# Performance work log

Hardware: AMD Instinct MI355X
Metric: run time of the kernel (lower is better)

The kernel has to match this reference:

```python
import jax, jax.numpy as jnp
import numpy as np
jax.config.update("jax_enable_x64", True)

N_ITER = 5
B, N = 64, 128

_C1 = jnp.uint64(0x9E3779B97F4A7C15)
_C2 = jnp.uint64(0xBF58476D1CE4E5B9)
_C3 = jnp.uint64(0x94D049BB133111EB)
_SALT = jnp.uint64(0xD1B54A32D192ED03)


def _mix(x):
    # splitmix64 finalizer: a bijection on uint64 -> preserves label equality classes
    z = x + _C1
    z = (z ^ (z >> jnp.uint64(30))) * _C2
    z = (z ^ (z >> jnp.uint64(27))) * _C3
    return z ^ (z >> jnp.uint64(31))


def setup_inputs() -> dict:
    key = jax.random.key(0)
    k1, k2 = jax.random.split(key)
    u = jax.random.uniform(k1, (B, N, N))
    adj = jnp.where(u < 0.06, 1.0, 0.0).astype(jnp.float32)
    adj = jnp.maximum(adj, jnp.transpose(adj, (0, 2, 1)))  # symmetric
    eye = jnp.eye(N, dtype=jnp.float32)
    adj = adj * (1.0 - eye)  # no self loops
    labels = jax.random.randint(k2, (B, N), 0, 10, dtype=jnp.int32)
    return {"adj": adj, "labels": labels}


def _kernel_contrib(h):
    # h: [B, N] uint64 labels. K[i,j] = #{(u,v): label_u == label_v}
    L = h.reshape(-1)                                   # [T]
    eq = (L[:, None] == L[None, :]).astype(jnp.float32)  # [T, T]
    return eq.reshape(B, N, B, N).sum(axis=(1, 3))       # [B, B]


def reference(adj, labels):
    adj_u = (adj > 0.5).astype(jnp.uint64)        # [B, N, N]
    h = _mix(labels.astype(jnp.uint64))           # initial labels (bijective relabel)
    K = _kernel_contrib(h)
    for _ in range(N_ITER):
        # commutative multiset hash of neighbor labels
        nsum = jnp.einsum('bij,bj->bi', adj_u, _mix(h ^ _SALT))
        # combine own label with neighbor multiset -> WL relabel
        h = _mix(_mix(h) + nsum)
        K = K + _kernel_contrib(h)
    d = jnp.sqrt(jnp.diag(K))
    return K / (d[:, None] * d[None, :])
```

## Files before the change

### kernel.cpp

```cpp
#include <hip/hip_runtime.h>

typedef unsigned long long u64;
typedef unsigned int u32;

#define NB 64
#define NN 128
#define NITER 5
#define NGEN 6
#define SALT 0xD1B54A32D192ED03ULL
#define NPAIR_OFF (NB*(NB-1)/2)
#define TSLOTS 256

__device__ __forceinline__ u64 mix64(u64 x) {
    u64 z = x + 0x9E3779B97F4A7C15ULL;
    z = (z ^ (z >> 30)) * 0xBF58476D1CE4E5B9ULL;
    z = (z ^ (z >> 27)) * 0x94D049BB133111EBULL;
    return z ^ (z >> 31);
}

__global__ __launch_bounds__(512) void wl_stage1(const float* __restrict__ adj,
                                                 const int* __restrict__ labels,
                                                 u64* __restrict__ hgen,
                                                 u64* __restrict__ keysg,
                                                 u32* __restrict__ cntsg,
                                                 float* __restrict__ Kpart,
                                                 float* __restrict__ out) {
    const int blk = blockIdx.x;
    const int t = threadIdx.x;
    const int u = t & 127;
    const int q = t >> 7;
    const bool writer = blk < NB;
    const int b    = writer ? blk   : (blk - NB) / NGEN;
    const int gent = writer ? NITER : (blk - NB) % NGEN;

    __shared__ u64 gsh[NN];
    __shared__ u64 psum[3][NN];
    __shared__ u64 keys[TSLOTS];
    __shared__ u32 cnts[TSLOTS];
    __shared__ u32 part[4];

    u32 m = 0;
    if (gent > 0) {
        const float* rowp = adj + ((size_t)b * NN + u) * NN + q * 32;
        #pragma unroll
        for (int k = 0; k < 8; ++k) {
            const float4 v = *(const float4*)(rowp + 4 * k);
            m |= (v.x > 0.5f ? 1u : 0u) << (4 * k);
            m |= (v.y > 0.5f ? 1u : 0u) << (4 * k + 1);
            m |= (v.z > 0.5f ? 1u : 0u) << (4 * k + 2);
            m |= (v.w > 0.5f ? 1u : 0u) << (4 * k + 3);
        }
    }

    u64 h = 0;
    if (q == 0) {
        h = mix64((u64)(u32)labels[b * NN + u]);
        if (writer) hgen[(size_t)b * (NGEN * NN) + u] = h;
    }

    for (int it = 0; it < gent; ++it) {
        if (q == 0) gsh[u] = mix64(h ^ SALT);
        __syncthreads();
        u64 s = 0;
        {
            u32 mm = m;
            const u64* gp = gsh + q * 32;
            while (mm) { int j = __builtin_ctz(mm); mm &= mm - 1; s += gp[j]; }
        }
        if (q) psum[q - 1][u] = s;
        __syncthreads();
        if (q == 0) {
            h = mix64(mix64(h) + s + psum[0][u] + psum[1][u] + psum[2][u]);
            if (writer) hgen[(size_t)b * (NGEN * NN) + (it + 1) * NN + u] = h;
        }
    }
    if (writer) return;

    if (t < TSLOTS) { keys[t] = 0ULL; cnts[t] = 0u; }
    __syncthreads();
    if (q == 0) {
        u32 s = (u32)h & (TSLOTS - 1);
        for (;;) {
            u64 old = atomicCAS((unsigned long long*)&keys[s], 0ULL, h);
            if (old == 0ULL || old == h) { atomicAdd(&cnts[s], 1u); break; }
            s = (s + 1) & (TSLOTS - 1);
        }
    }
    __syncthreads();

    const int bg = b * NGEN + gent;
    if (t < TSLOTS) {
        const u64 kk = keys[t];
        const u32 cc = cnts[t];
        keysg[(size_t)bg * TSLOTS + t] = kk;
        cntsg[(size_t)bg * TSLOTS + t] = cc;
        u32 acc = cc * cc;
        #pragma unroll
        for (int off = 32; off > 0; off >>= 1) acc += __shfl_down(acc, off);
        if ((t & 63) == 0) part[t >> 6] = acc;
    }
    __syncthreads();
    if (t == 0) {
        Kpart[bg] = (float)(part[0] + part[1] + part[2] + part[3]);
        if (gent == 0) out[b * NB + b] = 1.0f;
    }
}

__global__ __launch_bounds__(256) void wl_pairs(const u64* __restrict__ hgen,
                                                const u64* __restrict__ keysg,
                                                const u32* __restrict__ cntsg,
                                                const float* __restrict__ Kpart,
                                                float* __restrict__ out) {
    const int p = blockIdx.x;
    int b1 = (int)((1.0f + sqrtf(1.0f + 8.0f * (float)p)) * 0.5f);
    while (b1 * (b1 - 1) / 2 > p) --b1;
    while ((b1 + 1) * b1 / 2 <= p) ++b1;
    const int b2 = p - b1 * (b1 - 1) / 2;

    const int t = threadIdx.x;
    __shared__ u64 keys[NGEN * TSLOTS];
    __shared__ u32 cnts[NGEN * TSLOTS];
    __shared__ u32 part[4];
    __shared__ float dred[2 * NGEN];

    if (t < 2 * NGEN)
        dred[t] = Kpart[(t < NGEN ? b1 : b2) * NGEN + (t % NGEN)];

    {
        const ulonglong2* src = (const ulonglong2*)(keysg + (size_t)b2 * NGEN * TSLOTS);
        ulonglong2* dst = (ulonglong2*)keys;
        #pragma unroll
        for (int k = 0; k < 3; ++k) dst[t + 256 * k] = src[t + 256 * k];
    }
    {
        const uint4* src = (const uint4*)(cntsg + (size_t)b2 * NGEN * TSLOTS);
        uint4* dst = (uint4*)cnts;
        #pragma unroll
        for (int k = 0; k < 2; ++k) {
            const int idx = t + 256 * k;
            if (idx < 384) dst[idx] = src[idx];
        }
    }
    __syncthreads();

    u32 c = 0;
    const u64* abase = hgen + (size_t)b1 * NGEN * NN;
    #pragma unroll
    for (int k = 0; k < 3; ++k) {
        const int idx = t + 256 * k;
        const u64 a = abase[idx];
        const int base = (idx >> 7) * TSLOTS;
        u32 s = (u32)a & (TSLOTS - 1);
        for (;;) {
            const u64 kk = keys[base + s];
            if (kk == a) { c += cnts[base + s]; break; }
            if (kk == 0ULL) break;
            s = (s + 1) & (TSLOTS - 1);
        }
    }

    #pragma unroll
    for (int off = 32; off > 0; off >>= 1) c += __shfl_down(c, off);
    if ((t & 63) == 0) part[t >> 6] = c;
    __syncthreads();
    if (t == 0) {
        float d1 = 0.f, d2 = 0.f;
        #pragma unroll
        for (int g = 0; g < NGEN; ++g) { d1 += dred[g]; d2 += dred[NGEN + g]; }
        const float v = (float)(part[0] + part[1] + part[2] + part[3])
                      / (sqrtf(d1) * sqrtf(d2));
        out[b1 * NB + b2] = v;
        out[b2 * NB + b1] = v;
    }
}

extern "C" void kernel_launch(void* const* d_in, const int* in_sizes, int n_in,
                              void* d_out, int out_size, void* d_ws, size_t ws_size,
                              hipStream_t stream) {
    const float* adj   = (const float*)d_in[0];
    const int*  labels = (const int*)d_in[1];
    float* out = (float*)d_out;

    char* ws = (char*)d_ws;
    u64*   hgen  = (u64*)ws;
    float* Kpart = (float*)(ws + 448 * 1024);
    u64*   keysg = (u64*)(ws + 512 * 1024);
    u32*   cntsg = (u32*)(ws + 1536 * 1024);

    wl_stage1<<<NB + NB * NGEN, 512, 0, stream>>>(adj, labels, hgen, keysg,
                                                  cntsg, Kpart, out);
    wl_pairs <<<NPAIR_OFF, 256, 0, stream>>>(hgen, keysg, cntsg, Kpart, out);
}
```

Before: 27.86 us.

## Pair two graphs per block, use 32-bit labels and packed hash tables

Drops the separate writer blocks; each generation block now emits 32-bit truncated labels and a packed (key,count) table. The pairs kernel handles two b1 graphs against one loaded b2 table, halving table loads per pair. Adjacency bitmasks are built with wave ballots into shared memory. Truncating hashes to 32 bits adds a small collision risk relative to the 64-bit reference.

```diff
diff --git a/kernel.cpp b/kernel.cpp
--- a/kernel.cpp
+++ b/kernel.cpp
@@ -8,7 +8,6 @@
 #define NITER 5
 #define NGEN 6
 #define SALT 0xD1B54A32D192ED03ULL
-#define NPAIR_OFF (NB*(NB-1)/2)
 #define TSLOTS 256
 
 __device__ __forceinline__ u64 mix64(u64 x) {
@@ -18,159 +17,175 @@
     return z ^ (z >> 31);
 }
 
-__global__ __launch_bounds__(512) void wl_stage1(const float* __restrict__ adj,
-                                                 const int* __restrict__ labels,
-                                                 u64* __restrict__ hgen,
-                                                 u64* __restrict__ keysg,
-                                                 u32* __restrict__ cntsg,
-                                                 float* __restrict__ Kpart,
-                                                 float* __restrict__ out) {
+__global__ __launch_bounds__(512) void wl_gen(const float* __restrict__ adj,
+                                              const int* __restrict__ labels,
+                                              uint2* __restrict__ tabg,
+                                              u32* __restrict__ labels32,
+                                              float* __restrict__ Kpart,
+                                              float* __restrict__ out) {
     const int blk = blockIdx.x;
+    const int b   = blk / NGEN;
+    const int gen = blk % NGEN;
     const int t = threadIdx.x;
+    const int wave = t >> 6;
+    const int lane = t & 63;
     const int u = t & 127;
     const int q = t >> 7;
-    const bool writer = blk < NB;
-    const int b    = writer ? blk   : (blk - NB) / NGEN;
-    const int gent = writer ? NITER : (blk - NB) % NGEN;
-
+
+    __shared__ u64 bits_sh[NN][2];
     __shared__ u64 gsh[NN];
     __shared__ u64 psum[3][NN];
-    __shared__ u64 keys[TSLOTS];
+    __shared__ u32 keys[TSLOTS];
     __shared__ u32 cnts[TSLOTS];
-    __shared__ u32 part[4];
-
-    u32 m = 0;
-    if (gent > 0) {
-        const float* rowp = adj + ((size_t)b * NN + u) * NN + q * 32;
-        #pragma unroll
-        for (int k = 0; k < 8; ++k) {
-            const float4 v = *(const float4*)(rowp + 4 * k);
-            m |= (v.x > 0.5f ? 1u : 0u) << (4 * k);
-            m |= (v.y > 0.5f ? 1u : 0u) << (4 * k + 1);
-            m |= (v.z > 0.5f ? 1u : 0u) << (4 * k + 2);
-            m |= (v.w > 0.5f ? 1u : 0u) << (4 * k + 3);
-        }
-    }
-
-    u64 h = 0;
-    if (q == 0) {
-        h = mix64((u64)(u32)labels[b * NN + u]);
-        if (writer) hgen[(size_t)b * (NGEN * NN) + u] = h;
-    }
-
-    for (int it = 0; it < gent; ++it) {
+    __shared__ u32 part[8];
+
+    if (gen > 0) {
+        const float* abase = adj + (size_t)b * NN * NN;
+        #pragma unroll
+        for (int k = 0; k < 16; ++k) {
+            const int row = wave * 16 + k;
+            const float* arow = abase + (size_t)row * NN;
+            u64 m0 = __ballot(arow[lane] > 0.5f);
+            u64 m1 = __ballot(arow[64 + lane] > 0.5f);
+            if (lane == 0) { bits_sh[row][0] = m0; bits_sh[row][1] = m1; }
+        }
+    }
+    if (t < TSLOTS) { keys[t] = 0u; cnts[t] = 0u; }
+
+    u64 h = mix64((u64)(u32)labels[b * NN + u]);
+    __syncthreads();
+
+    u32 qm = 0;
+    if (gen > 0) qm = (u32)(bits_sh[u][q >> 1] >> ((q & 1) * 32));
+
+    for (int it = 0; it < gen; ++it) {
         if (q == 0) gsh[u] = mix64(h ^ SALT);
         __syncthreads();
         u64 s = 0;
         {
-            u32 mm = m;
+            u32 mm = qm;
             const u64* gp = gsh + q * 32;
             while (mm) { int j = __builtin_ctz(mm); mm &= mm - 1; s += gp[j]; }
         }
         if (q) psum[q - 1][u] = s;
         __syncthreads();
-        if (q == 0) {
-            h = mix64(mix64(h) + s + psum[0][u] + psum[1][u] + psum[2][u]);
-            if (writer) hgen[(size_t)b * (NGEN * NN) + (it + 1) * NN + u] = h;
-        }
-    }
-    if (writer) return;
-
-    if (t < TSLOTS) { keys[t] = 0ULL; cnts[t] = 0u; }
-    __syncthreads();
+        if (q == 0) h = mix64(mix64(h) + s + psum[0][u] + psum[1][u] + psum[2][u]);
+    }
+
     if (q == 0) {
-        u32 s = (u32)h & (TSLOTS - 1);
+        const u32 key = (u32)h;
+        u32 s = key & (TSLOTS - 1);
         for (;;) {
-            u64 old = atomicCAS((unsigned long long*)&keys[s], 0ULL, h);
-            if (old == 0ULL || old == h) { atomicAdd(&cnts[s], 1u); break; }
+            u32 old = atomicCAS(&keys[s], 0u, key);
+            if (old == 0u || old == key) { atomicAdd(&cnts[s], 1u); break; }
             s = (s + 1) & (TSLOTS - 1);
         }
     }
     __syncthreads();
 
-    const int bg = b * NGEN + gent;
     if (t < TSLOTS) {
-        const u64 kk = keys[t];
+        const u32 kk = keys[t];
         const u32 cc = cnts[t];
-        keysg[(size_t)bg * TSLOTS + t] = kk;
-        cntsg[(size_t)bg * TSLOTS + t] = cc;
+        tabg[(size_t)blk * TSLOTS + t] = make_uint2(kk, cc);
         u32 acc = cc * cc;
         #pragma unroll
         for (int off = 32; off > 0; off >>= 1) acc += __shfl_down(acc, off);
         if ((t & 63) == 0) part[t >> 6] = acc;
     }
+    if (t < NN) labels32[(size_t)blk * NN + t] = (u32)h;
     __syncthreads();
     if (t == 0) {
-        Kpart[bg] = (float)(part[0] + part[1] + part[2] + part[3]);
-        if (gent == 0) out[b * NB + b] = 1.0f;
-    }
-}
-
-__global__ __launch_bounds__(256) void wl_pairs(const u64* __restrict__ hgen,
-                                                const u64* __restrict__ keysg,
-                                                const u32* __restrict__ cntsg,
+        Kpart[blk] = (float)(part[0] + part[1] + part[2] + part[3]);
+        if (gen == 0) out[b * NB + b] = 1.0f;
+    }
+}
+
+__global__ __launch_bounds__(256) void wl_pairs(const uint2* __restrict__ tabg,
+                                                const u32* __restrict__ labels32,
                                                 const float* __restrict__ Kpart,
                                                 float* __restrict__ out) {
     const int p = blockIdx.x;
-    int b1 = (int)((1.0f + sqrtf(1.0f + 8.0f * (float)p)) * 0.5f);
-    while (b1 * (b1 - 1) / 2 > p) --b1;
-    while ((b1 + 1) * b1 / 2 <= p) ++b1;
-    const int b2 = p - b1 * (b1 - 1) / 2;
+    const int b2 = p >> 5;
+    const int i  = p & 31;
+    const int b1a = b2 + 1 + 2 * i;
+    if (b1a > 63) return;
+    const int b1b = b1a + 1;
+    const bool hasB = (b1b <= 63);
 
     const int t = threadIdx.x;
-    __shared__ u64 keys[NGEN * TSLOTS];
-    __shared__ u32 cnts[NGEN * TSLOTS];
-    __shared__ u32 part[4];
-    __shared__ float dred[2 * NGEN];
-
-    if (t < 2 * NGEN)
-        dred[t] = Kpart[(t < NGEN ? b1 : b2) * NGEN + (t % NGEN)];
-
+    __shared__ uint2 tab[NGEN * TSLOTS];
+    __shared__ u32 red[8];
+    __shared__ float dsh[3 * NGEN];
+
+    if (t < 3 * NGEN) {
+        const int which = t / NGEN;
+        const int g = t % NGEN;
+        const int bb = (which == 0) ? b2 : (which == 1) ? b1a : (hasB ? b1b : b1a);
+        dsh[t] = Kpart[bb * NGEN + g];
+    }
     {
-        const ulonglong2* src = (const ulonglong2*)(keysg + (size_t)b2 * NGEN * TSLOTS);
-        ulonglong2* dst = (ulonglong2*)keys;
+        const uint4* src = (const uint4*)(tabg + (size_t)b2 * NGEN * TSLOTS);
+        uint4* dst = (uint4*)tab;
         #pragma unroll
         for (int k = 0; k < 3; ++k) dst[t + 256 * k] = src[t + 256 * k];
     }
-    {
-        const uint4* src = (const uint4*)(cntsg + (size_t)b2 * NGEN * TSLOTS);
-        uint4* dst = (uint4*)cnts;
-        #pragma unroll
-        for (int k = 0; k < 2; ++k) {
-            const int idx = t + 256 * k;
-            if (idx < 384) dst[idx] = src[idx];
-        }
-    }
-    __syncthreads();
-
-    u32 c = 0;
-    const u64* abase = hgen + (size_t)b1 * NGEN * NN;
+    __syncthreads();
+
+    u32 ca = 0, cb = 0;
+    const u32* la = labels32 + (size_t)b1a * (NGEN * NN);
     #pragma unroll
     for (int k = 0; k < 3; ++k) {
         const int idx = t + 256 * k;
-        const u64 a = abase[idx];
         const int base = (idx >> 7) * TSLOTS;
-        u32 s = (u32)a & (TSLOTS - 1);
+        const u32 a = la[idx];
+        u32 s = a & (TSLOTS - 1);
         for (;;) {
-            const u64 kk = keys[base + s];
-            if (kk == a) { c += cnts[base + s]; break; }
-            if (kk == 0ULL) break;
+            const uint2 kv = tab[base + s];
+            if (kv.x == a) { ca += kv.y; break; }
+            if (kv.x == 0u) break;
             s = (s + 1) & (TSLOTS - 1);
         }
     }
+    if (hasB) {
+        const u32* lb = labels32 + (size_t)b1b * (NGEN * NN);
+        #pragma unroll
+        for (int k = 0; k < 3; ++k) {
+            const int idx = t + 256 * k;
+            const int base = (idx >> 7) * TSLOTS;
+            const u32 a = lb[idx];
+            u32 s = a & (TSLOTS - 1);
+            for (;;) {
+                const uint2 kv = tab[base + s];
+                if (kv.x == a) { cb += kv.y; break; }
+                if (kv.x == 0u) break;
+                s = (s + 1) & (TSLOTS - 1);
+            }
+        }
+    }
 
     #pragma unroll
-    for (int off = 32; off > 0; off >>= 1) c += __shfl_down(c, off);
-    if ((t & 63) == 0) part[t >> 6] = c;
+    for (int off = 32; off > 0; off >>= 1) {
+        ca += __shfl_down(ca, off);
+        cb += __shfl_down(cb, off);
+    }
+    if ((t & 63) == 0) { red[t >> 6] = ca; red[4 + (t >> 6)] = cb; }
     __syncthreads();
     if (t == 0) {
-        float d1 = 0.f, d2 = 0.f;
-        #pragma unroll
-        for (int g = 0; g < NGEN; ++g) { d1 += dred[g]; d2 += dred[NGEN + g]; }
-        const float v = (float)(part[0] + part[1] + part[2] + part[3])
-                      / (sqrtf(d1) * sqrtf(d2));
-        out[b1 * NB + b2] = v;
-        out[b2 * NB + b1] = v;
+        float d2s = 0.f, d1a = 0.f, d1b = 0.f;
+        #pragma unroll
+        for (int g = 0; g < NGEN; ++g) {
+            d2s += dsh[g]; d1a += dsh[NGEN + g]; d1b += dsh[2 * NGEN + g];
+        }
+        const float va = (float)(red[0] + red[1] + red[2] + red[3])
+                       / (sqrtf(d1a) * sqrtf(d2s));
+        out[b1a * NB + b2] = va;
+        out[b2 * NB + b1a] = va;
+        if (hasB) {
+            const float vb = (float)(red[4] + red[5] + red[6] + red[7])
+                           / (sqrtf(d1b) * sqrtf(d2s));
+            out[b1b * NB + b2] = vb;
+            out[b2 * NB + b1b] = vb;
+        }
     }
 }
 
@@ -182,12 +197,10 @@
     float* out = (float*)d_out;
 
     char* ws = (char*)d_ws;
-    u64*   hgen  = (u64*)ws;
-    float* Kpart = (float*)(ws + 448 * 1024);
-    u64*   keysg = (u64*)(ws + 512 * 1024);
-    u32*   cntsg = (u32*)(ws + 1536 * 1024);
-
-    wl_stage1<<<NB + NB * NGEN, 512, 0, stream>>>(adj, labels, hgen, keysg,
-                                                  cntsg, Kpart, out);
-    wl_pairs <<<NPAIR_OFF, 256, 0, stream>>>(hgen, keysg, cntsg, Kpart, out);
-}
+    uint2* tabg     = (uint2*)ws;
+    u32*   labels32 = (u32*)(ws + 1024 * 1024);
+    float* Kpart    = (float*)(ws + 1536 * 1024);
+
+    wl_gen  <<<NB * NGEN, 512, 0, stream>>>(adj, labels, tabg, labels32, Kpart, out);
+    wl_pairs<<<NB * 32,   256, 0, stream>>>(tabg, labels32, Kpart, out);
+}
```

Measured after the change: 32.70 us. +17.4%, slower.
